# Optimization experiments

Measured on AMD Instinct MI355X. Metric: run time of the kernel, lower is better.

Reference implementation:

```python
import jax, jax.numpy as jnp
import numpy as np

NUM_TRUE = 8
NUM_NULL = 2
NUM_EXPERTS = NUM_TRUE + NUM_NULL
TOP_K = 2


def setup_inputs() -> dict:
    key = jax.random.key(0)
    k0, k1, k2 = jax.random.split(key, 3)
    B, S, D = 4, 2048, 1024
    inputs = jax.random.normal(k0, (B, S, D), dtype=jnp.float32)
    gate_w = jax.random.normal(k1, (NUM_EXPERTS, D), dtype=jnp.float32) * 0.02
    gate_b = jnp.zeros((NUM_EXPERTS,), dtype=jnp.float32)
    # expert_w stored as [E, D_in, D_out] so expert i computes x @ expert_w[i] + expert_b[i]
    expert_w = jax.random.normal(k2, (NUM_TRUE, D, D), dtype=jnp.float32) * 0.02
    expert_b = jnp.zeros((NUM_TRUE, D), dtype=jnp.float32)
    return {"inputs": inputs, "gate_w": gate_w, "gate_b": gate_b,
            "expert_w": expert_w, "expert_b": expert_b}


def reference(inputs, gate_w, gate_b, expert_w, expert_b):
    D = inputs.shape[-1]
    x = inputs.reshape(-1, D)                       # [T, D]
    gate_logits = x @ gate_w.T + gate_b             # [T, E]
    gate_probs = jax.nn.softmax(gate_logits, axis=-1)
    weights, selected = jax.lax.top_k(gate_probs, TOP_K)  # [T, K]
    true_mask = selected < NUM_TRUE                 # null experts contribute nothing
    true_weights = weights * true_mask
    denom = true_weights.sum(axis=-1, keepdims=True)
    denom = jnp.where(denom > 0, denom, jnp.ones_like(denom))
    norm_w = (true_weights / denom).astype(x.dtype)  # [T, K]
    # per-(token, true-expert) combine weight; zero for unselected experts
    one_hot = jax.nn.one_hot(selected, NUM_EXPERTS, dtype=norm_w.dtype)  # [T, K, E]
    combine_w = jnp.einsum('tk,tke->te', norm_w, one_hot)[:, :NUM_TRUE]  # [T, E_true]
    # dense expert evaluation, then weighted combine (zero weights cancel
    # exactly as the gather/scatter loop in the torch code)
    expert_out = jnp.einsum('td,edh->teh', x, expert_w) + expert_b[None, :, :]  # [T, E_true, D]
    out = jnp.einsum('te,teh->th', combine_w, expert_out)  # [T, D]
    return out.reshape(inputs.shape[:-1] + (out.shape[-1],))
```

## Files before the change

### kernel.cpp

```cpp
#include <hip/hip_runtime.h>
#include <hip/hip_bf16.h>
#include <stdint.h>

#define T_TOKENS 8192
#define D_DIM    1024
#define NE       10
#define NT       8
#define SEG      2048

typedef unsigned short u16;
typedef __attribute__((ext_vector_type(8))) __bf16 bf16x8;
typedef __attribute__((ext_vector_type(4))) float  f32x4;
typedef __attribute__((ext_vector_type(8))) unsigned short u16x8;
typedef __attribute__((ext_vector_type(4))) unsigned short u16x4;

static __device__ __forceinline__ u16 f32_to_bf16(float f) {
  union { float f; uint32_t u; } v; v.f = f;
  uint32_t u = v.u;
  return (u16)((u + 0x7fffu + ((u >> 16) & 1u)) >> 16);
}
static __device__ __forceinline__ float bf16_to_f32(u16 u) {
  union { uint32_t u; float f; } v; v.u = ((uint32_t)u) << 16; return v.f;
}

static __device__ __forceinline__ void async_load16(const u16* g, u16* l) {
  __builtin_amdgcn_global_load_lds(
      (const __attribute__((address_space(1))) void*)(const void*)g,
      (__attribute__((address_space(3))) void*)(void*)l, 16, 0, 0);
}

union PrepShared {
  struct { float gws[NE * D_DIM]; float gbs[NE]; int se[16]; float swt[16]; } g;
  struct { float tile[64][68]; } t;
};

__global__ __launch_bounds__(256) void prep_kernel(
    const float* __restrict__ x, const float* __restrict__ gw,
    const float* __restrict__ gb, const float* __restrict__ W,
    u16* __restrict__ xb, u16* __restrict__ wT,
    int* __restrict__ cnt, int* __restrict__ tokList,
    int* __restrict__ revIdx, float* __restrict__ revW) {
  __shared__ PrepShared sh;
  int tid = threadIdx.x;

  if (blockIdx.x >= 1024) {
    int tb = blockIdx.x - 1024;
    int e  = tb >> 8;
    int rem = tb & 255;
    int k0 = (rem >> 4) * 64;
    int n0 = (rem & 15) * 64;
    int cr = tid & 15;
    int r0 = tid >> 4;
    const float* We = W + ((size_t)e << 20);
#pragma unroll
    for (int pass = 0; pass < 4; ++pass) {
      int r = pass * 16 + r0;
      f32x4 v = *(const f32x4*)&We[(size_t)(k0 + r) * 1024 + n0 + cr * 4];
#pragma unroll
      for (int j = 0; j < 4; ++j) sh.t.tile[cr * 4 + j][r] = v[j];
    }
    __syncthreads();
    u16* wTe = wT + ((size_t)e << 20);
#pragma unroll
    for (int pass = 0; pass < 4; ++pass) {
      int n = pass * 16 + r0;
      f32x4 tv = *(const f32x4*)&sh.t.tile[n][cr * 4];
      u16x4 pk;
#pragma unroll
      for (int j = 0; j < 4; ++j) pk[j] = f32_to_bf16(tv[j]);
      *(u16x4*)&wTe[(size_t)(n0 + n) * 1024 + k0 + cr * 4] = pk;
    }
    return;
  }

  {
    const f32x4* g4 = (const f32x4*)gw;
    f32x4* s4 = (f32x4*)sh.g.gws;
    for (int i = tid; i < NE * D_DIM / 4; i += 256) s4[i] = g4[i];
  }
  if (tid < NE) sh.g.gbs[tid] = gb[tid];
  __syncthreads();
  int lane = tid & 63;
  int wv   = tid >> 6;
  const f32x4* gws4 = (const f32x4*)sh.g.gws;
  for (int it = 0; it < 2; ++it) {
    int slot = wv * 2 + it;
    int t = blockIdx.x * 8 + slot;
    const f32x4* xr4 = (const f32x4*)(x + (size_t)t * D_DIM);
    f32x4 xv[4];
#pragma unroll
    for (int jj = 0; jj < 4; ++jj) xv[jj] = xr4[lane + 64 * jj];
    u16x4* xbr = (u16x4*)(xb + (size_t)t * D_DIM);
#pragma unroll
    for (int jj = 0; jj < 4; ++jj) {
      u16x4 pk;
#pragma unroll
      for (int k = 0; k < 4; ++k) pk[k] = f32_to_bf16(xv[jj][k]);
      xbr[lane + 64 * jj] = pk;
    }
    float logit[NE];
#pragma unroll
    for (int e = 0; e < NE; ++e) {
      float a = 0.f;
#pragma unroll
      for (int jj = 0; jj < 4; ++jj) {
        f32x4 gv = gws4[e * 256 + lane + 64 * jj];
#pragma unroll
        for (int k = 0; k < 4; ++k) a = fmaf(xv[jj][k], gv[k], a);
      }
#pragma unroll
      for (int off = 32; off >= 1; off >>= 1) a += __shfl_xor(a, off);
      logit[e] = a + sh.g.gbs[e];
    }
    float mx = logit[0];
#pragma unroll
    for (int e = 1; e < NE; ++e) mx = fmaxf(mx, logit[e]);
    float p[NE]; float s = 0.f;
#pragma unroll
    for (int e = 0; e < NE; ++e) { p[e] = expf(logit[e] - mx); s += p[e]; }
    int e0 = 0; float b0 = p[0];
#pragma unroll
    for (int e = 1; e < NE; ++e) if (p[e] > b0) { b0 = p[e]; e0 = e; }
    int e1 = -1; float b1 = -1.f;
#pragma unroll
    for (int e = 0; e < NE; ++e) if (e != e0 && p[e] > b1) { b1 = p[e]; e1 = e; }
    float w0 = b0 / s, w1 = b1 / s;
    float tw0 = (e0 < NT) ? w0 : 0.f;
    float tw1 = (e1 < NT) ? w1 : 0.f;
    float denom = tw0 + tw1;
    float nw0 = 0.f, nw1 = 0.f;
    if (denom > 0.f) { nw0 = tw0 / denom; nw1 = tw1 / denom; }
    if (lane == 0) {
      sh.g.se[slot * 2]     = (e0 < NT) ? e0 : -1;  sh.g.swt[slot * 2]     = nw0;
      sh.g.se[slot * 2 + 1] = (e1 < NT) ? e1 : -1;  sh.g.swt[slot * 2 + 1] = nw1;
      if (e0 >= NT) { revIdx[t * 2]     = -1; revW[t * 2]     = 0.f; }
      if (e1 >= NT) { revIdx[t * 2 + 1] = -1; revW[t * 2 + 1] = 0.f; }
    }
  }
  __syncthreads();
  if (tid < NT) {
    int e = tid, c = 0;
    for (int i = 0; i < 16; ++i) c += (sh.g.se[i] == e);
    if (c > 0) {
      int base = atomicAdd(&cnt[e * 32], c);
      int j = 0;
      for (int i = 0; i < 16; ++i) {
        if (sh.g.se[i] == e) {
          int tt  = blockIdx.x * 8 + (i >> 1);
          int pos = base + j;
          tokList[e * SEG + pos]   = tt;
          revIdx[tt * 2 + (i & 1)] = e * SEG + pos;
          revW[tt * 2 + (i & 1)]   = sh.g.swt[i];
          ++j;
        }
      }
    }
  }
}

__global__ __launch_bounds__(512, 4) void moe_gemm(
    const u16* __restrict__ xb, const u16* __restrict__ wT,
    const int* __restrict__ cnt, const int* __restrict__ tokList,
    const float* __restrict__ eb, u16* __restrict__ ybuf) {
  int e  = blockIdx.x;
  int c  = cnt[e * 32];
  int m0 = blockIdx.z * 256;
  if (m0 >= c) return;
  int n0 = blockIdx.y * 128;
  __shared__ __align__(16) u16 As[3][256 * 32];
  __shared__ __align__(16) u16 Bs[3][128 * 32];
  __shared__ int tokS[256];
  int tid = threadIdx.x;
  if (tid < 256) {
    int gm = m0 + tid;
    tokS[tid] = (gm < c) ? tokList[e * SEG + gm] : tokList[e * SEG];
  }
  __syncthreads();
  int lane = tid & 63;
  int wv   = tid >> 6;
  int rl  = lane >> 2;
  int kcp = lane & 3;
  int kcd = kcp ^ ((rl >> 1) & 3);
  int rowA0 = wv * 32 + rl, rowA1 = rowA0 + 16;
  int rowB  = wv * 16 + rl;
  const u16* gA0 = xb + (size_t)tokS[rowA0] * 1024 + kcd * 8;
  const u16* gA1 = xb + (size_t)tokS[rowA1] * 1024 + kcd * 8;
  const u16* wTe = wT + ((size_t)e << 20);
  const u16* gB0 = wTe + (size_t)(n0 + rowB) * 1024 + kcd * 8;
  int ldsA0 = (wv * 32) * 32, ldsA1 = ldsA0 + 16 * 32, ldsB0 = (wv * 16) * 32;

  int wm = wv >> 2, wn = wv & 3;
  int lrow = lane & 15;
  int q    = lane >> 4;
  int sw   = (q ^ ((lrow >> 1) & 3)) * 8;
  f32x4 acc[8][2];
#pragma unroll
  for (int i = 0; i < 8; ++i)
#pragma unroll
    for (int j = 0; j < 2; ++j) acc[i][j] = (f32x4){0.f, 0.f, 0.f, 0.f};

#pragma unroll
  for (int p = 0; p < 2; ++p) {
    int ko = p * 32;
    async_load16(gA0 + ko, As[p] + ldsA0);
    async_load16(gA1 + ko, As[p] + ldsA1);
    async_load16(gB0 + ko, Bs[p] + ldsB0);
  }

  int cur = 0;
  for (int kt = 0; kt < 32; ++kt) {
    asm volatile("s_barrier" ::: "memory");
    if (kt < 30) {
      int st = cur - 1; if (st < 0) st += 3;
      int ko = (kt + 2) * 32;
      async_load16(gA0 + ko, As[st] + ldsA0);
      async_load16(gA1 + ko, As[st] + ldsA1);
      async_load16(gB0 + ko, Bs[st] + ldsB0);
      asm volatile("s_waitcnt vmcnt(6)" ::: "memory");
    } else if (kt == 30) {
      asm volatile("s_waitcnt vmcnt(3)" ::: "memory");
    } else {
      asm volatile("s_waitcnt vmcnt(0)" ::: "memory");
    }
    asm volatile("s_barrier" ::: "memory");
    bf16x8 bfr[2];
#pragma unroll
    for (int nt = 0; nt < 2; ++nt)
      bfr[nt] = *(const bf16x8*)(Bs[cur] + (wn * 32 + nt * 16 + lrow) * 32 + sw);
#pragma unroll
    for (int mt = 0; mt < 8; ++mt) {
      bf16x8 af = *(const bf16x8*)(As[cur] + (wm * 128 + mt * 16 + lrow) * 32 + sw);
#pragma unroll
      for (int nt = 0; nt < 2; ++nt)
        acc[mt][nt] = __builtin_amdgcn_mfma_f32_16x16x32_bf16(
            af, bfr[nt], acc[mt][nt], 0, 0, 0);
    }
    ++cur; if (cur == 3) cur = 0;
  }
  int rq = lane >> 4;
  float bias[2];
#pragma unroll
  for (int nt = 0; nt < 2; ++nt)
    bias[nt] = eb[e * 1024 + n0 + wn * 32 + nt * 16 + lrow];
  u16* yb = ybuf + ((size_t)(e * SEG + m0)) * 1024 + n0 + wn * 32 + lrow;
#pragma unroll
  for (int mt = 0; mt < 8; ++mt) {
#pragma unroll
    for (int r = 0; r < 4; ++r) {
      int ml = wm * 128 + mt * 16 + rq * 4 + r;
      u16* row = yb + (size_t)ml * 1024;
#pragma unroll
      for (int nt = 0; nt < 2; ++nt)
        row[nt * 16] = f32_to_bf16(acc[mt][nt][r] + bias[nt]);
    }
  }
}

__global__ __launch_bounds__(256) void combine_kernel(
    const u16* __restrict__ ybuf, const int* __restrict__ revIdx,
    const float* __restrict__ revW, float* __restrict__ out) {
  int tid = threadIdx.x, lane = tid & 63, wv = tid >> 6;
  int t  = blockIdx.x * 4 + wv;
  int i0 = revIdx[t * 2], i1 = revIdx[t * 2 + 1];
  float w0 = revW[t * 2], w1 = revW[t * 2 + 1];
  float o[16];
#pragma unroll
  for (int k = 0; k < 16; ++k) o[k] = 0.f;
  if (i0 >= 0) {
    const u16x8* y = (const u16x8*)(ybuf + (size_t)i0 * 1024);
#pragma unroll
    for (int jj = 0; jj < 2; ++jj) {
      u16x8 v = y[lane + 64 * jj];
#pragma unroll
      for (int k = 0; k < 8; ++k) o[jj * 8 + k] += w0 * bf16_to_f32(v[k]);
    }
  }
  if (i1 >= 0) {
    const u16x8* y = (const u16x8*)(ybuf + (size_t)i1 * 1024);
#pragma unroll
    for (int jj = 0; jj < 2; ++jj) {
      u16x8 v = y[lane + 64 * jj];
#pragma unroll
      for (int k = 0; k < 8; ++k) o[jj * 8 + k] += w1 * bf16_to_f32(v[k]);
    }
  }
  f32x4* o4 = (f32x4*)(out + (size_t)t * 1024);
#pragma unroll
  for (int jj = 0; jj < 2; ++jj)
#pragma unroll
    for (int h = 0; h < 2; ++h) {
      f32x4 vv = {o[jj * 8 + h * 4], o[jj * 8 + h * 4 + 1],
                  o[jj * 8 + h * 4 + 2], o[jj * 8 + h * 4 + 3]};
      __builtin_nontemporal_store(vv, &o4[2 * (lane + 64 * jj) + h]);
    }
}

extern "C" void kernel_launch(void* const* d_in, const int* in_sizes, int n_in,
                              void* d_out, int out_size, void* d_ws, size_t ws_size,
                              hipStream_t stream) {
  const float* x  = (const float*)d_in[0];
  const float* gw = (const float*)d_in[1];
  const float* gb = (const float*)d_in[2];
  const float* ew = (const float*)d_in[3];
  const float* eb = (const float*)d_in[4];
  float* out = (float*)d_out;
  char* ws = (char*)d_ws;
  int*   cnt     = (int*)ws;
  int*   tokList = (int*)(ws + 4096);
  int*   revIdx  = (int*)(ws + 4096 + 65536);
  float* revW    = (float*)(ws + 4096 + 131072);
  u16*   xb      = (u16*)(ws + 200704);
  u16*   wT      = (u16*)(ws + 200704 + 16777216);
  u16*   ybuf    = (u16*)(ws + 200704 + 33554432);

  hipMemsetAsync(cnt, 0, 4096, stream);
  prep_kernel<<<3072, 256, 0, stream>>>(x, gw, gb, ew, xb, wT, cnt, tokList,
                                        revIdx, revW);
  moe_gemm<<<dim3(8, 8, 8), 512, 0, stream>>>(xb, wT, cnt, tokList, eb, ybuf);
  combine_kernel<<<2048, 256, 0, stream>>>(ybuf, revIdx, revW, out);
}
```

Before: 175.5 us.

## Fuse prep, GEMM and combine into one persistent cooperative kernel

Merges the three kernels (routing/convert, expert GEMM, combine) into a single cooperative kernel of 256 blocks of 512 threads, using grid.sync between phases. Each block handles 32 tokens of routing, 8 weight-transpose tiles, two GEMM tile assignments and 32 tokens of combine. This is meant to remove launch gaps and tail effects between kernels. In exchange the grid is limited to 256 blocks, which caps GEMM occupancy and parallelism, and the grid-wide barriers add their own cost.

```diff
diff --git a/kernel.cpp b/kernel.cpp
--- a/kernel.cpp
+++ b/kernel.cpp
@@ -1,6 +1,9 @@
 #include <hip/hip_runtime.h>
+#include <hip/hip_cooperative_groups.h>
 #include <hip/hip_bf16.h>
 #include <stdint.h>
+
+namespace cg = cooperative_groups;
 
 #define T_TOKENS 8192
 #define D_DIM    1024
@@ -29,124 +32,100 @@
       (__attribute__((address_space(3))) void*)(void*)l, 16, 0, 0);
 }
 
-union PrepShared {
-  struct { float gws[NE * D_DIM]; float gbs[NE]; int se[16]; float swt[16]; } g;
-  struct { float tile[64][68]; } t;
+union __align__(16) FusedShared {
+  struct { u16 As[3][256 * 32]; u16 Bs[3][128 * 32]; int tokS[256]; } m;
+  struct { float gws[NE * D_DIM]; float gbs[NE]; int se[64]; float swt[64]; } g;
+  struct { float tile[64][65]; } t;
 };
 
-__global__ __launch_bounds__(256) void prep_kernel(
+__global__ __launch_bounds__(512) void fused_moe(
     const float* __restrict__ x, const float* __restrict__ gw,
     const float* __restrict__ gb, const float* __restrict__ W,
-    u16* __restrict__ xb, u16* __restrict__ wT,
+    const float* __restrict__ eb, u16* __restrict__ xb, u16* __restrict__ wT,
     int* __restrict__ cnt, int* __restrict__ tokList,
-    int* __restrict__ revIdx, float* __restrict__ revW) {
-  __shared__ PrepShared sh;
-  int tid = threadIdx.x;
-
-  if (blockIdx.x >= 1024) {
-    int tb = blockIdx.x - 1024;
-    int e  = tb >> 8;
-    int rem = tb & 255;
-    int k0 = (rem >> 4) * 64;
-    int n0 = (rem & 15) * 64;
-    int cr = tid & 15;
-    int r0 = tid >> 4;
-    const float* We = W + ((size_t)e << 20);
-#pragma unroll
-    for (int pass = 0; pass < 4; ++pass) {
-      int r = pass * 16 + r0;
-      f32x4 v = *(const f32x4*)&We[(size_t)(k0 + r) * 1024 + n0 + cr * 4];
-#pragma unroll
-      for (int j = 0; j < 4; ++j) sh.t.tile[cr * 4 + j][r] = v[j];
-    }
-    __syncthreads();
-    u16* wTe = wT + ((size_t)e << 20);
-#pragma unroll
-    for (int pass = 0; pass < 4; ++pass) {
-      int n = pass * 16 + r0;
-      f32x4 tv = *(const f32x4*)&sh.t.tile[n][cr * 4];
-      u16x4 pk;
-#pragma unroll
-      for (int j = 0; j < 4; ++j) pk[j] = f32_to_bf16(tv[j]);
-      *(u16x4*)&wTe[(size_t)(n0 + n) * 1024 + k0 + cr * 4] = pk;
-    }
-    return;
-  }
+    int* __restrict__ revIdx, float* __restrict__ revW,
+    u16* __restrict__ ybuf, float* __restrict__ out) {
+  __shared__ FusedShared sh;
+  cg::grid_group grid = cg::this_grid();
+  int tid  = threadIdx.x;
+  int bx   = blockIdx.x;
+  int lane = tid & 63;
+  int wv   = tid >> 6;
 
   {
     const f32x4* g4 = (const f32x4*)gw;
     f32x4* s4 = (f32x4*)sh.g.gws;
-    for (int i = tid; i < NE * D_DIM / 4; i += 256) s4[i] = g4[i];
-  }
-  if (tid < NE) sh.g.gbs[tid] = gb[tid];
+    for (int i = tid; i < NE * D_DIM / 4; i += 512) s4[i] = g4[i];
+    if (tid < NE) sh.g.gbs[tid] = gb[tid];
+  }
   __syncthreads();
-  int lane = tid & 63;
-  int wv   = tid >> 6;
-  const f32x4* gws4 = (const f32x4*)sh.g.gws;
-  for (int it = 0; it < 2; ++it) {
-    int slot = wv * 2 + it;
-    int t = blockIdx.x * 8 + slot;
-    const f32x4* xr4 = (const f32x4*)(x + (size_t)t * D_DIM);
-    f32x4 xv[4];
-#pragma unroll
-    for (int jj = 0; jj < 4; ++jj) xv[jj] = xr4[lane + 64 * jj];
-    u16x4* xbr = (u16x4*)(xb + (size_t)t * D_DIM);
-#pragma unroll
-    for (int jj = 0; jj < 4; ++jj) {
-      u16x4 pk;
-#pragma unroll
-      for (int k = 0; k < 4; ++k) pk[k] = f32_to_bf16(xv[jj][k]);
-      xbr[lane + 64 * jj] = pk;
-    }
-    float logit[NE];
-#pragma unroll
-    for (int e = 0; e < NE; ++e) {
-      float a = 0.f;
+  {
+    const f32x4* gws4 = (const f32x4*)sh.g.gws;
+    for (int it = 0; it < 4; ++it) {
+      int slot = wv * 4 + it;
+      int t = bx * 32 + slot;
+      const f32x4* xr4 = (const f32x4*)(x + (size_t)t * D_DIM);
+      f32x4 xv[4];
+#pragma unroll
+      for (int jj = 0; jj < 4; ++jj) xv[jj] = xr4[lane + 64 * jj];
+      u16x4* xbr = (u16x4*)(xb + (size_t)t * D_DIM);
 #pragma unroll
       for (int jj = 0; jj < 4; ++jj) {
-        f32x4 gv = gws4[e * 256 + lane + 64 * jj];
-#pragma unroll
-        for (int k = 0; k < 4; ++k) a = fmaf(xv[jj][k], gv[k], a);
-      }
-#pragma unroll
-      for (int off = 32; off >= 1; off >>= 1) a += __shfl_xor(a, off);
-      logit[e] = a + sh.g.gbs[e];
-    }
-    float mx = logit[0];
-#pragma unroll
-    for (int e = 1; e < NE; ++e) mx = fmaxf(mx, logit[e]);
-    float p[NE]; float s = 0.f;
-#pragma unroll
-    for (int e = 0; e < NE; ++e) { p[e] = expf(logit[e] - mx); s += p[e]; }
-    int e0 = 0; float b0 = p[0];
-#pragma unroll
-    for (int e = 1; e < NE; ++e) if (p[e] > b0) { b0 = p[e]; e0 = e; }
-    int e1 = -1; float b1 = -1.f;
-#pragma unroll
-    for (int e = 0; e < NE; ++e) if (e != e0 && p[e] > b1) { b1 = p[e]; e1 = e; }
-    float w0 = b0 / s, w1 = b1 / s;
-    float tw0 = (e0 < NT) ? w0 : 0.f;
-    float tw1 = (e1 < NT) ? w1 : 0.f;
-    float denom = tw0 + tw1;
-    float nw0 = 0.f, nw1 = 0.f;
-    if (denom > 0.f) { nw0 = tw0 / denom; nw1 = tw1 / denom; }
-    if (lane == 0) {
-      sh.g.se[slot * 2]     = (e0 < NT) ? e0 : -1;  sh.g.swt[slot * 2]     = nw0;
-      sh.g.se[slot * 2 + 1] = (e1 < NT) ? e1 : -1;  sh.g.swt[slot * 2 + 1] = nw1;
-      if (e0 >= NT) { revIdx[t * 2]     = -1; revW[t * 2]     = 0.f; }
-      if (e1 >= NT) { revIdx[t * 2 + 1] = -1; revW[t * 2 + 1] = 0.f; }
+        u16x4 pk;
+#pragma unroll
+        for (int k = 0; k < 4; ++k) pk[k] = f32_to_bf16(xv[jj][k]);
+        xbr[lane + 64 * jj] = pk;
+      }
+      float logit[NE];
+#pragma unroll
+      for (int e = 0; e < NE; ++e) {
+        float a = 0.f;
+#pragma unroll
+        for (int jj = 0; jj < 4; ++jj) {
+          f32x4 gv = gws4[e * 256 + lane + 64 * jj];
+#pragma unroll
+          for (int k = 0; k < 4; ++k) a = fmaf(xv[jj][k], gv[k], a);
+        }
+#pragma unroll
+        for (int off = 32; off >= 1; off >>= 1) a += __shfl_xor(a, off);
+        logit[e] = a + sh.g.gbs[e];
+      }
+      float mx = logit[0];
+#pragma unroll
+      for (int e = 1; e < NE; ++e) mx = fmaxf(mx, logit[e]);
+      float p[NE]; float s = 0.f;
+#pragma unroll
+      for (int e = 0; e < NE; ++e) { p[e] = expf(logit[e] - mx); s += p[e]; }
+      int e0 = 0; float b0 = p[0];
+#pragma unroll
+      for (int e = 1; e < NE; ++e) if (p[e] > b0) { b0 = p[e]; e0 = e; }
+      int e1 = -1; float b1 = -1.f;
+#pragma unroll
+      for (int e = 0; e < NE; ++e) if (e != e0 && p[e] > b1) { b1 = p[e]; e1 = e; }
+      float w0 = b0 / s, w1 = b1 / s;
+      float tw0 = (e0 < NT) ? w0 : 0.f;
+      float tw1 = (e1 < NT) ? w1 : 0.f;
+      float denom = tw0 + tw1;
+      float nw0 = 0.f, nw1 = 0.f;
+      if (denom > 0.f) { nw0 = tw0 / denom; nw1 = tw1 / denom; }
+      if (lane == 0) {
+        sh.g.se[slot * 2]     = (e0 < NT) ? e0 : -1;  sh.g.swt[slot * 2]     = nw0;
+        sh.g.se[slot * 2 + 1] = (e1 < NT) ? e1 : -1;  sh.g.swt[slot * 2 + 1] = nw1;
+        if (e0 >= NT) { revIdx[t * 2]     = -1; revW[t * 2]     = 0.f; }
+        if (e1 >= NT) { revIdx[t * 2 + 1] = -1; revW[t * 2 + 1] = 0.f; }
+      }
     }
   }
   __syncthreads();
   if (tid < NT) {
     int e = tid, c = 0;
-    for (int i = 0; i < 16; ++i) c += (sh.g.se[i] == e);
+    for (int i = 0; i < 64; ++i) c += (sh.g.se[i] == e);
     if (c > 0) {
       int base = atomicAdd(&cnt[e * 32], c);
       int j = 0;
-      for (int i = 0; i < 16; ++i) {
+      for (int i = 0; i < 64; ++i) {
         if (sh.g.se[i] == e) {
-          int tt  = blockIdx.x * 8 + (i >> 1);
+          int tt  = bx * 32 + (i >> 1);
           int pos = base + j;
           tokList[e * SEG + pos]   = tt;
           revIdx[tt * 2 + (i & 1)] = e * SEG + pos;
@@ -156,143 +135,171 @@
       }
     }
   }
-}
-
-__global__ __launch_bounds__(512, 4) void moe_gemm(
-    const u16* __restrict__ xb, const u16* __restrict__ wT,
-    const int* __restrict__ cnt, const int* __restrict__ tokList,
-    const float* __restrict__ eb, u16* __restrict__ ybuf) {
-  int e  = blockIdx.x;
-  int c  = cnt[e * 32];
-  int m0 = blockIdx.z * 256;
-  if (m0 >= c) return;
-  int n0 = blockIdx.y * 128;
-  __shared__ __align__(16) u16 As[3][256 * 32];
-  __shared__ __align__(16) u16 Bs[3][128 * 32];
-  __shared__ int tokS[256];
-  int tid = threadIdx.x;
-  if (tid < 256) {
-    int gm = m0 + tid;
-    tokS[tid] = (gm < c) ? tokList[e * SEG + gm] : tokList[e * SEG];
-  }
-  __syncthreads();
-  int lane = tid & 63;
-  int wv   = tid >> 6;
-  int rl  = lane >> 2;
-  int kcp = lane & 3;
-  int kcd = kcp ^ ((rl >> 1) & 3);
-  int rowA0 = wv * 32 + rl, rowA1 = rowA0 + 16;
-  int rowB  = wv * 16 + rl;
-  const u16* gA0 = xb + (size_t)tokS[rowA0] * 1024 + kcd * 8;
-  const u16* gA1 = xb + (size_t)tokS[rowA1] * 1024 + kcd * 8;
-  const u16* wTe = wT + ((size_t)e << 20);
-  const u16* gB0 = wTe + (size_t)(n0 + rowB) * 1024 + kcd * 8;
-  int ldsA0 = (wv * 32) * 32, ldsA1 = ldsA0 + 16 * 32, ldsB0 = (wv * 16) * 32;
-
-  int wm = wv >> 2, wn = wv & 3;
-  int lrow = lane & 15;
-  int q    = lane >> 4;
-  int sw   = (q ^ ((lrow >> 1) & 3)) * 8;
-  f32x4 acc[8][2];
-#pragma unroll
-  for (int i = 0; i < 8; ++i)
-#pragma unroll
-    for (int j = 0; j < 2; ++j) acc[i][j] = (f32x4){0.f, 0.f, 0.f, 0.f};
-
-#pragma unroll
-  for (int p = 0; p < 2; ++p) {
-    int ko = p * 32;
-    async_load16(gA0 + ko, As[p] + ldsA0);
-    async_load16(gA1 + ko, As[p] + ldsA1);
-    async_load16(gB0 + ko, Bs[p] + ldsB0);
-  }
-
-  int cur = 0;
-  for (int kt = 0; kt < 32; ++kt) {
-    asm volatile("s_barrier" ::: "memory");
-    if (kt < 30) {
-      int st = cur - 1; if (st < 0) st += 3;
-      int ko = (kt + 2) * 32;
-      async_load16(gA0 + ko, As[st] + ldsA0);
-      async_load16(gA1 + ko, As[st] + ldsA1);
-      async_load16(gB0 + ko, Bs[st] + ldsB0);
-      asm volatile("s_waitcnt vmcnt(6)" ::: "memory");
-    } else if (kt == 30) {
-      asm volatile("s_waitcnt vmcnt(3)" ::: "memory");
-    } else {
-      asm volatile("s_waitcnt vmcnt(0)" ::: "memory");
-    }
-    asm volatile("s_barrier" ::: "memory");
-    bf16x8 bfr[2];
-#pragma unroll
-    for (int nt = 0; nt < 2; ++nt)
-      bfr[nt] = *(const bf16x8*)(Bs[cur] + (wn * 32 + nt * 16 + lrow) * 32 + sw);
-#pragma unroll
-    for (int mt = 0; mt < 8; ++mt) {
-      bf16x8 af = *(const bf16x8*)(As[cur] + (wm * 128 + mt * 16 + lrow) * 32 + sw);
+
+  {
+    int cr = tid & 15;
+    int rr = tid >> 4;
+    for (int ti = 0; ti < 8; ++ti) {
+      __syncthreads();
+      int gid = bx * 8 + ti;
+      int e   = gid >> 8;
+      int rem = gid & 255;
+      int k0  = (rem >> 4) * 64;
+      int n0  = (rem & 15) * 64;
+      const float* We = W + ((size_t)e << 20);
+#pragma unroll
+      for (int pass = 0; pass < 2; ++pass) {
+        int r = pass * 32 + rr;
+        f32x4 v = *(const f32x4*)&We[(size_t)(k0 + r) * 1024 + n0 + cr * 4];
+#pragma unroll
+        for (int j = 0; j < 4; ++j) sh.t.tile[cr * 4 + j][r] = v[j];
+      }
+      __syncthreads();
+      u16* wTe = wT + ((size_t)e << 20);
+#pragma unroll
+      for (int pass = 0; pass < 2; ++pass) {
+        int n = pass * 32 + rr;
+        u16x4 pk;
+#pragma unroll
+        for (int j = 0; j < 4; ++j) pk[j] = f32_to_bf16(sh.t.tile[n][cr * 4 + j]);
+        *(u16x4*)&wTe[(size_t)(n0 + n) * 1024 + k0 + cr * 4] = pk;
+      }
+    }
+  }
+
+  grid.sync();
+
+  {
+    int rl  = lane >> 2;
+    int kcp = lane & 3;
+    int kcd = kcp ^ ((rl >> 1) & 3);
+    int wm = wv >> 2, wn = wv & 3;
+    int lrow = lane & 15;
+    int q    = lane >> 4;
+    int sw   = (q ^ ((lrow >> 1) & 3)) * 8;
+    int rq   = lane >> 4;
+    for (int rep = 0; rep < 2; ++rep) {
+      __syncthreads();
+      int asg = bx + rep * 256;
+      int e   = asg & 7;
+      int ny  = (asg >> 3) & 7;
+      int mz  = asg >> 6;
+      int c   = cnt[e * 32];
+      int m0  = mz * 256;
+      if (m0 >= c) continue;
+      int n0  = ny * 128;
+      if (tid < 256) {
+        int gm = m0 + tid;
+        sh.m.tokS[tid] = (gm < c) ? tokList[e * SEG + gm] : tokList[e * SEG];
+      }
+      __syncthreads();
+      int rowA0 = wv * 32 + rl, rowA1 = rowA0 + 16;
+      int rowB  = wv * 16 + rl;
+      const u16* gA0 = xb + (size_t)sh.m.tokS[rowA0] * 1024 + kcd * 8;
+      const u16* gA1 = xb + (size_t)sh.m.tokS[rowA1] * 1024 + kcd * 8;
+      const u16* wTe = wT + ((size_t)e << 20);
+      const u16* gB0 = wTe + (size_t)(n0 + rowB) * 1024 + kcd * 8;
+      int ldsA0 = (wv * 32) * 32, ldsA1 = ldsA0 + 16 * 32, ldsB0 = (wv * 16) * 32;
+
+      f32x4 acc[8][2];
+#pragma unroll
+      for (int i = 0; i < 8; ++i)
+#pragma unroll
+        for (int j = 0; j < 2; ++j) acc[i][j] = (f32x4){0.f, 0.f, 0.f, 0.f};
+
+#pragma unroll
+      for (int p = 0; p < 2; ++p) {
+        int ko = p * 32;
+        async_load16(gA0 + ko, sh.m.As[p] + ldsA0);
+        async_load16(gA1 + ko, sh.m.As[p] + ldsA1);
+        async_load16(gB0 + ko, sh.m.Bs[p] + ldsB0);
+      }
+      int cur = 0;
+      for (int kt = 0; kt < 32; ++kt) {
+        asm volatile("s_barrier" ::: "memory");
+        if (kt < 30) {
+          int st = cur - 1; if (st < 0) st += 3;
+          int ko = (kt + 2) * 32;
+          async_load16(gA0 + ko, sh.m.As[st] + ldsA0);
+          async_load16(gA1 + ko, sh.m.As[st] + ldsA1);
+          async_load16(gB0 + ko, sh.m.Bs[st] + ldsB0);
+          asm volatile("s_waitcnt vmcnt(6)" ::: "memory");
+        } else if (kt == 30) {
+          asm volatile("s_waitcnt vmcnt(3)" ::: "memory");
+        } else {
+          asm volatile("s_waitcnt vmcnt(0)" ::: "memory");
+        }
+        asm volatile("s_barrier" ::: "memory");
+        bf16x8 bfr[2];
+#pragma unroll
+        for (int nt = 0; nt < 2; ++nt)
+          bfr[nt] = *(const bf16x8*)(sh.m.Bs[cur] + (wn * 32 + nt * 16 + lrow) * 32 + sw);
+#pragma unroll
+        for (int mt = 0; mt < 8; ++mt) {
+          bf16x8 af = *(const bf16x8*)(sh.m.As[cur] + (wm * 128 + mt * 16 + lrow) * 32 + sw);
+#pragma unroll
+          for (int nt = 0; nt < 2; ++nt)
+            acc[mt][nt] = __builtin_amdgcn_mfma_f32_16x16x32_bf16(
+                af, bfr[nt], acc[mt][nt], 0, 0, 0);
+        }
+        ++cur; if (cur == 3) cur = 0;
+      }
+      float bias[2];
 #pragma unroll
       for (int nt = 0; nt < 2; ++nt)
-        acc[mt][nt] = __builtin_amdgcn_mfma_f32_16x16x32_bf16(
-            af, bfr[nt], acc[mt][nt], 0, 0, 0);
-    }
-    ++cur; if (cur == 3) cur = 0;
-  }
-  int rq = lane >> 4;
-  float bias[2];
-#pragma unroll
-  for (int nt = 0; nt < 2; ++nt)
-    bias[nt] = eb[e * 1024 + n0 + wn * 32 + nt * 16 + lrow];
-  u16* yb = ybuf + ((size_t)(e * SEG + m0)) * 1024 + n0 + wn * 32 + lrow;
-#pragma unroll
-  for (int mt = 0; mt < 8; ++mt) {
-#pragma unroll
-    for (int r = 0; r < 4; ++r) {
-      int ml = wm * 128 + mt * 16 + rq * 4 + r;
-      u16* row = yb + (size_t)ml * 1024;
-#pragma unroll
-      for (int nt = 0; nt < 2; ++nt)
-        row[nt * 16] = f32_to_bf16(acc[mt][nt][r] + bias[nt]);
-    }
-  }
-}
-
-__global__ __launch_bounds__(256) void combine_kernel(
-    const u16* __restrict__ ybuf, const int* __restrict__ revIdx,
-    const float* __restrict__ revW, float* __restrict__ out) {
-  int tid = threadIdx.x, lane = tid & 63, wv = tid >> 6;
-  int t  = blockIdx.x * 4 + wv;
-  int i0 = revIdx[t * 2], i1 = revIdx[t * 2 + 1];
-  float w0 = revW[t * 2], w1 = revW[t * 2 + 1];
-  float o[16];
-#pragma unroll
-  for (int k = 0; k < 16; ++k) o[k] = 0.f;
-  if (i0 >= 0) {
-    const u16x8* y = (const u16x8*)(ybuf + (size_t)i0 * 1024);
-#pragma unroll
-    for (int jj = 0; jj < 2; ++jj) {
-      u16x8 v = y[lane + 64 * jj];
-#pragma unroll
-      for (int k = 0; k < 8; ++k) o[jj * 8 + k] += w0 * bf16_to_f32(v[k]);
-    }
-  }
-  if (i1 >= 0) {
-    const u16x8* y = (const u16x8*)(ybuf + (size_t)i1 * 1024);
-#pragma unroll
-    for (int jj = 0; jj < 2; ++jj) {
-      u16x8 v = y[lane + 64 * jj];
-#pragma unroll
-      for (int k = 0; k < 8; ++k) o[jj * 8 + k] += w1 * bf16_to_f32(v[k]);
-    }
-  }
-  f32x4* o4 = (f32x4*)(out + (size_t)t * 1024);
-#pragma unroll
-  for (int jj = 0; jj < 2; ++jj)
-#pragma unroll
-    for (int h = 0; h < 2; ++h) {
-      f32x4 vv = {o[jj * 8 + h * 4], o[jj * 8 + h * 4 + 1],
-                  o[jj * 8 + h * 4 + 2], o[jj * 8 + h * 4 + 3]};
-      __builtin_nontemporal_store(vv, &o4[2 * (lane + 64 * jj) + h]);
-    }
+        bias[nt] = eb[e * 1024 + n0 + wn * 32 + nt * 16 + lrow];
+      u16* yb = ybuf + ((size_t)(e * SEG + m0)) * 1024 + n0 + wn * 32 + lrow;
+#pragma unroll
+      for (int mt = 0; mt < 8; ++mt) {
+#pragma unroll
+        for (int r = 0; r < 4; ++r) {
+          int ml = wm * 128 + mt * 16 + rq * 4 + r;
+          u16* row = yb + (size_t)ml * 1024;
+#pragma unroll
+          for (int nt = 0; nt < 2; ++nt)
+            row[nt * 16] = f32_to_bf16(acc[mt][nt][r] + bias[nt]);
+        }
+      }
+    }
+  }
+
+  grid.sync();
+
+  for (int it = 0; it < 4; ++it) {
+    int t  = bx * 32 + wv * 4 + it;
+    int i0 = revIdx[t * 2], i1 = revIdx[t * 2 + 1];
+    float w0 = revW[t * 2], w1 = revW[t * 2 + 1];
+    float o[16];
+#pragma unroll
+    for (int k = 0; k < 16; ++k) o[k] = 0.f;
+    if (i0 >= 0) {
+      const u16x8* y = (const u16x8*)(ybuf + (size_t)i0 * 1024);
+#pragma unroll
+      for (int jj = 0; jj < 2; ++jj) {
+        u16x8 v = y[lane + 64 * jj];
+#pragma unroll
+        for (int k = 0; k < 8; ++k) o[jj * 8 + k] += w0 * bf16_to_f32(v[k]);
+      }
+    }
+    if (i1 >= 0) {
+      const u16x8* y = (const u16x8*)(ybuf + (size_t)i1 * 1024);
+#pragma unroll
+      for (int jj = 0; jj < 2; ++jj) {
+        u16x8 v = y[lane + 64 * jj];
+#pragma unroll
+        for (int k = 0; k < 8; ++k) o[jj * 8 + k] += w1 * bf16_to_f32(v[k]);
+      }
+    }
+    f32x4* o4 = (f32x4*)(out + (size_t)t * 1024);
+#pragma unroll
+    for (int jj = 0; jj < 2; ++jj)
+#pragma unroll
+      for (int h = 0; h < 2; ++h) {
+        f32x4 vv = {o[jj * 8 + h * 4], o[jj * 8 + h * 4 + 1],
+                    o[jj * 8 + h * 4 + 2], o[jj * 8 + h * 4 + 3]};
+        __builtin_nontemporal_store(vv, &o4[2 * (lane + 64 * jj) + h]);
+      }
+  }
 }
 
 extern "C" void kernel_launch(void* const* d_in, const int* in_sizes, int n_in,
@@ -314,8 +321,9 @@
   u16*   ybuf    = (u16*)(ws + 200704 + 33554432);
 
   hipMemsetAsync(cnt, 0, 4096, stream);
-  prep_kernel<<<3072, 256, 0, stream>>>(x, gw, gb, ew, xb, wT, cnt, tokList,
-                                        revIdx, revW);
-  moe_gemm<<<dim3(8, 8, 8), 512, 0, stream>>>(xb, wT, cnt, tokList, eb, ybuf);
-  combine_kernel<<<2048, 256, 0, stream>>>(ybuf, revIdx, revW, out);
-}
+  void* args[] = {(void*)&x, (void*)&gw, (void*)&gb, (void*)&ew, (void*)&eb,
+                  (void*)&xb, (void*)&wT, (void*)&cnt, (void*)&tokList,
+                  (void*)&revIdx, (void*)&revW, (void*)&ybuf, (void*)&out};
+  hipLaunchCooperativeKernel((const void*)fused_moe, dim3(256), dim3(512),
+                             args, 0, stream);
+}
```

Result: slower. 266.6 us (+51.9%).

## Enlarge MoE GEMM tile to 256x256 with BK=64 double buffering

Applied to the files above, without the earlier changes.

The expert GEMM block tile grows from 256x128 to 256x256 and the K step from 32 to 64, so the grid halves along N. The LDS pipeline goes from three stages to two, with a new XOR swizzle, and the MFMA phases are split into interleaved sub-steps wrapped in s_setprio. This raises arithmetic intensity and cuts redundant A-row gathers, but doubles accumulator registers and LDS use (128 KB), lowering occupancy. Because the grid is smaller, many tiles may be empty when expert token counts are uneven.

```diff
diff --git a/kernel.cpp b/kernel.cpp
--- a/kernel.cpp
+++ b/kernel.cpp
@@ -28,6 +28,7 @@
       (const __attribute__((address_space(1))) void*)(const void*)g,
       (__attribute__((address_space(3))) void*)(void*)l, 16, 0, 0);
 }
+
 
 union PrepShared {
   struct { float gws[NE * D_DIM]; float gbs[NE]; int se[16]; float swt[16]; } g;
@@ -158,7 +159,7 @@
   }
 }
 
-__global__ __launch_bounds__(512, 4) void moe_gemm(
+__global__ __launch_bounds__(512) void moe_gemm(
     const u16* __restrict__ xb, const u16* __restrict__ wT,
     const int* __restrict__ cnt, const int* __restrict__ tokList,
     const float* __restrict__ eb, u16* __restrict__ ybuf) {
@@ -166,9 +167,9 @@
   int c  = cnt[e * 32];
   int m0 = blockIdx.z * 256;
   if (m0 >= c) return;
-  int n0 = blockIdx.y * 128;
-  __shared__ __align__(16) u16 As[3][256 * 32];
-  __shared__ __align__(16) u16 Bs[3][128 * 32];
+  int n0 = blockIdx.y * 256;
+  __shared__ __align__(16) u16 As[2][256 * 64];
+  __shared__ __align__(16) u16 Bs[2][256 * 64];
   __shared__ int tokS[256];
   int tid = threadIdx.x;
   if (tid < 256) {
@@ -178,71 +179,115 @@
   __syncthreads();
   int lane = tid & 63;
   int wv   = tid >> 6;
-  int rl  = lane >> 2;
-  int kcp = lane & 3;
-  int kcd = kcp ^ ((rl >> 1) & 3);
-  int rowA0 = wv * 32 + rl, rowA1 = rowA0 + 16;
-  int rowB  = wv * 16 + rl;
-  const u16* gA0 = xb + (size_t)tokS[rowA0] * 1024 + kcd * 8;
-  const u16* gA1 = xb + (size_t)tokS[rowA1] * 1024 + kcd * 8;
+  int sub = lane >> 3;
+  int chd = (lane & 7) ^ sub;
+  const u16* gA[4];
+#pragma unroll
+  for (int j = 0; j < 4; ++j) {
+    int tok = tokS[wv * 32 + j * 8 + sub];
+    gA[j] = xb + (size_t)tok * 1024 + chd * 8;
+  }
   const u16* wTe = wT + ((size_t)e << 20);
-  const u16* gB0 = wTe + (size_t)(n0 + rowB) * 1024 + kcd * 8;
-  int ldsA0 = (wv * 32) * 32, ldsA1 = ldsA0 + 16 * 32, ldsB0 = (wv * 16) * 32;
+  const u16* gB  = wTe + (size_t)(n0 + wv * 32 + sub) * 1024 + chd * 8;
+  int ldsW = (wv * 32) * 64;
 
   int wm = wv >> 2, wn = wv & 3;
   int lrow = lane & 15;
   int q    = lane >> 4;
-  int sw   = (q ^ ((lrow >> 1) & 3)) * 8;
-  f32x4 acc[8][2];
+  int pk0 = ((q)     ^ (lrow & 7)) * 8;
+  int pk1 = ((4 + q) ^ (lrow & 7)) * 8;
+  f32x4 acc[8][4];
 #pragma unroll
   for (int i = 0; i < 8; ++i)
 #pragma unroll
-    for (int j = 0; j < 2; ++j) acc[i][j] = (f32x4){0.f, 0.f, 0.f, 0.f};
-
-#pragma unroll
-  for (int p = 0; p < 2; ++p) {
-    int ko = p * 32;
-    async_load16(gA0 + ko, As[p] + ldsA0);
-    async_load16(gA1 + ko, As[p] + ldsA1);
-    async_load16(gB0 + ko, Bs[p] + ldsB0);
+    for (int j = 0; j < 4; ++j) acc[i][j] = (f32x4){0.f, 0.f, 0.f, 0.f};
+
+#pragma unroll
+  for (int j = 0; j < 4; ++j) {
+    async_load16(gA[j], As[0] + ldsW + j * 512);
+    async_load16(gB + j * 8192, Bs[0] + ldsW + j * 512);
   }
 
   int cur = 0;
-  for (int kt = 0; kt < 32; ++kt) {
-    asm volatile("s_barrier" ::: "memory");
-    if (kt < 30) {
-      int st = cur - 1; if (st < 0) st += 3;
-      int ko = (kt + 2) * 32;
-      async_load16(gA0 + ko, As[st] + ldsA0);
-      async_load16(gA1 + ko, As[st] + ldsA1);
-      async_load16(gB0 + ko, Bs[st] + ldsB0);
-      asm volatile("s_waitcnt vmcnt(6)" ::: "memory");
-    } else if (kt == 30) {
-      asm volatile("s_waitcnt vmcnt(3)" ::: "memory");
+  for (int kt = 0; kt < 16; ++kt) {
+    asm volatile("s_barrier" ::: "memory");
+    if (kt < 15) {
+      int nx = cur ^ 1;
+      int ko = (kt + 1) * 64;
+#pragma unroll
+      for (int j = 0; j < 4; ++j) {
+        async_load16(gA[j] + ko, As[nx] + ldsW + j * 512);
+        async_load16(gB + j * 8192 + ko, Bs[nx] + ldsW + j * 512);
+      }
+      asm volatile("s_waitcnt vmcnt(8)" ::: "memory");
     } else {
       asm volatile("s_waitcnt vmcnt(0)" ::: "memory");
     }
     asm volatile("s_barrier" ::: "memory");
-    bf16x8 bfr[2];
-#pragma unroll
-    for (int nt = 0; nt < 2; ++nt)
-      bfr[nt] = *(const bf16x8*)(Bs[cur] + (wn * 32 + nt * 16 + lrow) * 32 + sw);
-#pragma unroll
-    for (int mt = 0; mt < 8; ++mt) {
-      bf16x8 af = *(const bf16x8*)(As[cur] + (wm * 128 + mt * 16 + lrow) * 32 + sw);
-#pragma unroll
-      for (int nt = 0; nt < 2; ++nt)
+    const u16* Ab = As[cur];
+    const u16* Bb = Bs[cur];
+    bf16x8 bfr[4], af[4];
+#pragma unroll
+    for (int nt = 0; nt < 4; ++nt)
+      bfr[nt] = *(const bf16x8*)(Bb + (wn * 64 + nt * 16 + lrow) * 64 + pk0);
+#pragma unroll
+    for (int mt = 0; mt < 4; ++mt)
+      af[mt] = *(const bf16x8*)(Ab + (wm * 128 + mt * 16 + lrow) * 64 + pk0);
+    __builtin_amdgcn_s_setprio(1);
+#pragma unroll
+    for (int mt = 0; mt < 4; ++mt)
+#pragma unroll
+      for (int nt = 0; nt < 4; ++nt)
         acc[mt][nt] = __builtin_amdgcn_mfma_f32_16x16x32_bf16(
-            af, bfr[nt], acc[mt][nt], 0, 0, 0);
-    }
-    ++cur; if (cur == 3) cur = 0;
+            af[mt], bfr[nt], acc[mt][nt], 0, 0, 0);
+    __builtin_amdgcn_s_setprio(0);
+    asm volatile("s_barrier" ::: "memory");
+#pragma unroll
+    for (int mt = 0; mt < 4; ++mt)
+      af[mt] = *(const bf16x8*)(Ab + (wm * 128 + (mt + 4) * 16 + lrow) * 64 + pk0);
+    __builtin_amdgcn_s_setprio(1);
+#pragma unroll
+    for (int mt = 0; mt < 4; ++mt)
+#pragma unroll
+      for (int nt = 0; nt < 4; ++nt)
+        acc[mt + 4][nt] = __builtin_amdgcn_mfma_f32_16x16x32_bf16(
+            af[mt], bfr[nt], acc[mt + 4][nt], 0, 0, 0);
+    __builtin_amdgcn_s_setprio(0);
+    asm volatile("s_barrier" ::: "memory");
+#pragma unroll
+    for (int nt = 0; nt < 4; ++nt)
+      bfr[nt] = *(const bf16x8*)(Bb + (wn * 64 + nt * 16 + lrow) * 64 + pk1);
+#pragma unroll
+    for (int mt = 0; mt < 4; ++mt)
+      af[mt] = *(const bf16x8*)(Ab + (wm * 128 + mt * 16 + lrow) * 64 + pk1);
+    __builtin_amdgcn_s_setprio(1);
+#pragma unroll
+    for (int mt = 0; mt < 4; ++mt)
+#pragma unroll
+      for (int nt = 0; nt < 4; ++nt)
+        acc[mt][nt] = __builtin_amdgcn_mfma_f32_16x16x32_bf16(
+            af[mt], bfr[nt], acc[mt][nt], 0, 0, 0);
+    __builtin_amdgcn_s_setprio(0);
+    asm volatile("s_barrier" ::: "memory");
+#pragma unroll
+    for (int mt = 0; mt < 4; ++mt)
+      af[mt] = *(const bf16x8*)(Ab + (wm * 128 + (mt + 4) * 16 + lrow) * 64 + pk1);
+    __builtin_amdgcn_s_setprio(1);
+#pragma unroll
+    for (int mt = 0; mt < 4; ++mt)
+#pragma unroll
+      for (int nt = 0; nt < 4; ++nt)
+        acc[mt + 4][nt] = __builtin_amdgcn_mfma_f32_16x16x32_bf16(
+            af[mt], bfr[nt], acc[mt + 4][nt], 0, 0, 0);
+    __builtin_amdgcn_s_setprio(0);
+    cur ^= 1;
   }
   int rq = lane >> 4;
-  float bias[2];
-#pragma unroll
-  for (int nt = 0; nt < 2; ++nt)
-    bias[nt] = eb[e * 1024 + n0 + wn * 32 + nt * 16 + lrow];
-  u16* yb = ybuf + ((size_t)(e * SEG + m0)) * 1024 + n0 + wn * 32 + lrow;
+  float bias[4];
+#pragma unroll
+  for (int nt = 0; nt < 4; ++nt)
+    bias[nt] = eb[e * 1024 + n0 + wn * 64 + nt * 16 + lrow];
+  u16* yb = ybuf + ((size_t)(e * SEG + m0)) * 1024 + n0 + wn * 64 + lrow;
 #pragma unroll
   for (int mt = 0; mt < 8; ++mt) {
 #pragma unroll
@@ -250,7 +295,7 @@
       int ml = wm * 128 + mt * 16 + rq * 4 + r;
       u16* row = yb + (size_t)ml * 1024;
 #pragma unroll
-      for (int nt = 0; nt < 2; ++nt)
+      for (int nt = 0; nt < 4; ++nt)
         row[nt * 16] = f32_to_bf16(acc[mt][nt][r] + bias[nt]);
     }
   }
@@ -316,6 +361,6 @@
   hipMemsetAsync(cnt, 0, 4096, stream);
   prep_kernel<<<3072, 256, 0, stream>>>(x, gw, gb, ew, xb, wT, cnt, tokList,
                                         revIdx, revW);
-  moe_gemm<<<dim3(8, 8, 8), 512, 0, stream>>>(xb, wT, cnt, tokList, eb, ybuf);
+  moe_gemm<<<dim3(8, 4, 8), 512, 0, stream>>>(xb, wT, cnt, tokList, eb, ybuf);
   combine_kernel<<<2048, 256, 0, stream>>>(ybuf, revIdx, revW, out);
 }
```

New measurement: 178.9 us. About the same (+1.9%).
